# Performance work log

Hardware: AMD Instinct MI355X
Metric: run time of the kernel (lower is better)

## Reference

```python
import jax, jax.numpy as jnp
import numpy as np

USER_NUM = 100000
ITEM_NUM = 50000
EMBED_DIM = 64
N_LAYERS = 2
NNZ_UU, NNZ_UI, NNZ_II = 1600000, 2000000, 800000


def setup_inputs() -> dict:
    key = jax.random.key(0)
    ks = jax.random.split(key, 11)
    return {
        "user_embedding": jax.random.normal(ks[0], (USER_NUM, EMBED_DIM), jnp.float32),
        "item_embedding": jax.random.normal(ks[1], (ITEM_NUM, EMBED_DIM), jnp.float32),
        "uu_val": jax.random.uniform(ks[2], (NNZ_UU,), jnp.float32),
        "ui_val": jax.random.uniform(ks[3], (NNZ_UI,), jnp.float32),
        "ii_val": jax.random.uniform(ks[4], (NNZ_II,), jnp.float32),
        "uu_rows": jax.random.randint(ks[5], (NNZ_UU,), 0, USER_NUM, jnp.int32),
        "uu_cols": jax.random.randint(ks[6], (NNZ_UU,), 0, USER_NUM, jnp.int32),
        "ui_rows": jax.random.randint(ks[7], (NNZ_UI,), 0, USER_NUM, jnp.int32),
        "ui_cols": jax.random.randint(ks[8], (NNZ_UI,), 0, ITEM_NUM, jnp.int32),
        "ii_rows": jax.random.randint(ks[9], (NNZ_II,), 0, ITEM_NUM, jnp.int32),
        "ii_cols": jax.random.randint(ks[10], (NNZ_II,), 0, ITEM_NUM, jnp.int32),
    }


def _spmm(rows, cols, vals, x, n_out):
    # sparse(COO) @ dense: gather source features, scale by edge value, scatter-add to rows
    return jax.ops.segment_sum(vals[:, None] * x[cols], rows, num_segments=n_out)


def reference(user_embedding, item_embedding, uu_val, ui_val, ii_val,
              uu_rows, uu_cols, ui_rows, ui_cols, ii_rows, ii_cols):
    u = user_embedding
    i = item_embedding
    # running sum for mean over (n_layers + 1) layer outputs
    u_sum, i_sum = u, i
    for _ in range(N_LAYERS):
        u_from_i = _spmm(ui_rows, ui_cols, ui_val, i, USER_NUM)        # user_item_graph @ item
        i_from_u = _spmm(ui_cols, ui_rows, ui_val, u, ITEM_NUM)        # user_item_graph.T @ user
        uu = _spmm(uu_rows, uu_cols, uu_val, u, USER_NUM)              # user_graph @ user
        ii = _spmm(ii_rows, ii_cols, ii_val, i, ITEM_NUM)              # item_graph @ item
        u = 0.5 * (uu + u_from_i)   # mean over stacked pair
        i = 0.5 * (ii + i_from_u)
        u_sum = u_sum + u
        i_sum = i_sum + i
    inv = 1.0 / (N_LAYERS + 1)
    return u_sum * inv, i_sum * inv
```

## Files before the change

kernel.cpp:

```cpp
#include <hip/hip_runtime.h>

typedef _Float16 half8_t __attribute__((ext_vector_type(8)));
typedef _Float16 half4_t __attribute__((ext_vector_type(4)));

#define NU 100000
#define NI 50000
#define NR (NU + NI)
#define D 64
#define COARSE 1024
#define RPB 147
#define CAP 8800
#define CHUNK 6144
#define RPT 6
#define RPT2 9
#define NT4 (NR * 16)
#define PKSLACK 448

__global__ void init_kernel(const float4* __restrict__ ue, const float4* __restrict__ ie,
                            half4_t* __restrict__ curh, int* __restrict__ tots) {
    int idx = blockIdx.x * 256 + threadIdx.x;
    if (idx < COARSE) tots[idx] = 0;
    if (idx >= NT4) return;
    float4 v = (idx < NU * 16) ? ue[idx] : ie[idx - NU * 16];
    half4_t h;
    h[0] = (_Float16)v.x; h[1] = (_Float16)v.y; h[2] = (_Float16)v.z; h[3] = (_Float16)v.w;
    curh[idx] = h;
}

__device__ __forceinline__ int place_dest(int p, const int* ui_r, const int* ui_c,
                                          const int* uu_r, const int* ii_r,
                                          int n_ui, int n_uu) {
    if (p < 2 * n_ui) {
        int e = p >> 1;
        return (p & 1) ? NU + ui_c[e] : ui_r[e];
    } else if (p < 2 * n_ui + n_uu) {
        return uu_r[p - 2 * n_ui];
    } else {
        return NU + ii_r[p - 2 * n_ui - n_uu];
    }
}

__global__ void count_kernel(const int* __restrict__ ui_r, const int* __restrict__ ui_c,
                             const int* __restrict__ uu_r, const int* __restrict__ ii_r,
                             int* __restrict__ tots, int n_ui, int n_uu, int nnzt) {
    __shared__ int cnt[COARSE];
    int tid = threadIdx.x;
    cnt[tid] = 0;
    __syncthreads();
    int blk0 = blockIdx.x * CHUNK;
#pragma unroll
    for (int k = 0; k < RPT; k++) {
        int p = blk0 + k * 1024 + tid;
        if (p < nnzt) {
            int dest = place_dest(p, ui_r, ui_c, uu_r, ii_r, n_ui, n_uu);
            atomicAdd(&cnt[dest / RPB], 1);
        }
    }
    __syncthreads();
    if (cnt[tid]) atomicAdd(&tots[tid], cnt[tid]);
}

__global__ void scan1_kernel(const int* __restrict__ tots, int* __restrict__ coarse_base,
                             int* __restrict__ cursor) {
    __shared__ int s[COARSE];
    int tid = threadIdx.x;
    int x = tots[tid];
    s[tid] = x;
    __syncthreads();
    for (int off = 1; off < COARSE; off <<= 1) {
        int t = (tid >= off) ? s[tid - off] : 0;
        __syncthreads();
        s[tid] += t;
        __syncthreads();
    }
    int excl = s[tid] - x;
    coarse_base[tid] = excl;
    cursor[tid] = excl;
    if (tid == COARSE - 1) coarse_base[COARSE] = s[tid];
}

__global__ void place_kernel(const int* __restrict__ ui_r, const int* __restrict__ ui_c,
                             const float* __restrict__ ui_v,
                             const int* __restrict__ uu_r, const int* __restrict__ uu_c,
                             const float* __restrict__ uu_v,
                             const int* __restrict__ ii_r, const int* __restrict__ ii_c,
                             const float* __restrict__ ii_v,
                             int* __restrict__ cursor, uint2* __restrict__ scratch,
                             int n_ui, int n_uu, int nnzt) {
    __shared__ uint2 rec[CHUNK];
    __shared__ int cnt[COARSE];
    __shared__ int lbase[COARSE];
    __shared__ int base_s[COARSE];
    __shared__ int s_ntot;
    int tid = threadIdx.x;
    cnt[tid] = 0;
    __syncthreads();
    int blk0 = blockIdx.x * CHUNK;
    unsigned rk[RPT];
    int sk[RPT];
    unsigned short vk[RPT];
#pragma unroll
    for (int k = 0; k < RPT; k++) {
        int p = blk0 + k * 1024 + tid;
        rk[k] = 0xFFFFFFFFu;
        if (p < nnzt) {
            int dest, src;
            float v;
            if (p < 2 * n_ui) {
                int e = p >> 1;
                int r = ui_r[e], cc = ui_c[e];
                v = ui_v[e];
                if (p & 1) { dest = NU + cc; src = r; }
                else       { dest = r; src = NU + cc; }
            } else if (p < 2 * n_ui + n_uu) {
                int e = p - 2 * n_ui;
                dest = uu_r[e]; src = uu_c[e]; v = uu_v[e];
            } else {
                int e = p - 2 * n_ui - n_uu;
                dest = NU + ii_r[e]; src = NU + ii_c[e]; v = ii_v[e];
            }
            int c = dest / RPB;
            int lr = atomicAdd(&cnt[c], 1);
            int dl = dest - c * RPB;
            rk[k] = ((unsigned)dl << 24) | ((unsigned)c << 14) | (unsigned)lr;
            sk[k] = src;
            _Float16 hv = (_Float16)v;
            __builtin_memcpy(&vk[k], &hv, 2);
        }
    }
    __syncthreads();
    int own = cnt[tid];
    if (own) base_s[tid] = atomicAdd(&cursor[tid], own);
    lbase[tid] = own;
    __syncthreads();
    for (int off = 1; off < COARSE; off <<= 1) {
        int t = (tid >= off) ? lbase[tid - off] : 0;
        __syncthreads();
        lbase[tid] += t;
        __syncthreads();
    }
    int incl = lbase[tid];
    __syncthreads();
    lbase[tid] = incl - own;
    if (tid == COARSE - 1) s_ntot = incl;
    __syncthreads();
#pragma unroll
    for (int k = 0; k < RPT; k++) {
        if (rk[k] == 0xFFFFFFFFu) continue;
        int c  = (rk[k] >> 14) & 0x3FF;
        int lr = rk[k] & 0x3FFF;
        int dl = rk[k] >> 24;
        rec[lbase[c] + lr] = make_uint2(((unsigned)dl << 18) | (unsigned)sk[k],
                                        ((unsigned)c << 16) | (unsigned)vk[k]);
    }
    __syncthreads();
    int ntot = s_ntot;
    for (int i = tid; i < ntot; i += 1024) {
        uint2 r = rec[i];
        int c = r.y >> 16;
        scratch[base_s[c] + (i - lbase[c])] = r;
    }
}

__global__ void csr_kernel(const uint2* __restrict__ scratch, const int* __restrict__ coarse_base,
                           int* __restrict__ ptr, int* __restrict__ pk_src,
                           unsigned short* __restrict__ pk_val) {
    __shared__ int s[1024];
    __shared__ int fine[256];
    __shared__ int fill[256];
    __shared__ int lsrc[CAP];
    __shared__ unsigned short lval[CAP];
    __shared__ int s_pn;
    int c = blockIdx.x, tid = threadIdx.x;
    int rbeg = c * RPB;
    int rcnt = NR - rbeg;
    if (rcnt > RPB) rcnt = RPB;
    if (rcnt < 0) rcnt = 0;
    int base = coarse_base[c], end = coarse_base[c + 1];
    int n = end - base;
    int pkc    = ((base + 3) & ~3) + c * PKSLACK;
    int pknext = ((end  + 3) & ~3) + (c + 1) * PKSLACK;
    bool small = (n <= RPT2 * 1024);
    if (tid < 256) fine[tid] = 0;
    __syncthreads();
    uint2 rc[RPT2];
    if (small) {
#pragma unroll
        for (int k = 0; k < RPT2; k++) {
            int i = k * 1024 + tid;
            if (i < n) {
                rc[k] = scratch[base + i];
                atomicAdd(&fine[rc[k].x >> 18], 1);
            }
        }
    } else {
        for (int i = tid; i < n; i += 1024)
            atomicAdd(&fine[scratch[base + i].x >> 18], 1);
    }
    __syncthreads();
    int own = (tid < 256) ? fine[tid] : 0;
    int own4 = (own + 3) & ~3;
    s[tid] = own4;
    __syncthreads();
    for (int off = 1; off < 256; off <<= 1) {
        int t = (tid >= off) ? s[tid - off] : 0;
        __syncthreads();
        s[tid] += t;
        __syncthreads();
    }
    int excl4 = s[tid] - own4;
    if (tid < rcnt) ptr[rbeg + tid] = pkc + excl4;
    if (tid == 0 && rbeg + rcnt == NR) ptr[NR] = pknext;
    if (tid < 256) fill[tid] = excl4;
    if (tid == 255) s_pn = s[255];
    __syncthreads();
    int pn = s_pn;
    if (small && pn <= CAP) {
        for (int i = tid; i < pn; i += 1024) { lsrc[i] = 0; lval[i] = 0; }
        __syncthreads();
#pragma unroll
        for (int k = 0; k < RPT2; k++) {
            int i = k * 1024 + tid;
            if (i < n) {
                int dl = rc[k].x >> 18;
                int slot = atomicAdd(&fill[dl], 1);
                lsrc[slot] = rc[k].x & 0x3FFFF;
                lval[slot] = (unsigned short)rc[k].y;
            }
        }
        __syncthreads();
        for (int i = tid; i < pn; i += 1024) {
            pk_src[pkc + i] = lsrc[i] << 7;
            pk_val[pkc + i] = lval[i];
        }
        for (int i = pkc + pn + tid; i < pknext; i += 1024) { pk_src[i] = 0; pk_val[i] = 0; }
    } else {
        for (int i = pkc + tid; i < pknext; i += 1024) { pk_src[i] = 0; pk_val[i] = 0; }
        __syncthreads();
        for (int i = tid; i < n; i += 1024) {
            uint2 r2 = scratch[base + i];
            int dl = r2.x >> 18;
            int slot = atomicAdd(&fill[dl], 1);
            pk_src[pkc + slot] = (r2.x & 0x3FFFF) << 7;
            pk_val[pkc + slot] = (unsigned short)r2.y;
        }
    }
}

template<int SV, int SX>
__device__ __forceinline__ void fmamix(float& a, unsigned v, unsigned x) {
    if constexpr (SV == 0 && SX == 0)
        asm("v_fma_mix_f32 %0, %1, %2, %0 op_sel:[0,0,0] op_sel_hi:[1,1,0]"
            : "+v"(a) : "v"(v), "v"(x));
    else if constexpr (SV == 0 && SX == 1)
        asm("v_fma_mix_f32 %0, %1, %2, %0 op_sel:[0,1,0] op_sel_hi:[1,1,0]"
            : "+v"(a) : "v"(v), "v"(x));
    else if constexpr (SV == 1 && SX == 0)
        asm("v_fma_mix_f32 %0, %1, %2, %0 op_sel:[1,0,0] op_sel_hi:[1,1,0]"
            : "+v"(a) : "v"(v), "v"(x));
    else
        asm("v_fma_mix_f32 %0, %1, %2, %0 op_sel:[1,1,0] op_sel_hi:[1,1,0]"
            : "+v"(a) : "v"(v), "v"(x));
}

template<int SV>
__device__ __forceinline__ void edge_fma(float (&acc)[8], unsigned vw, const uint4& x) {
    fmamix<SV, 0>(acc[0], vw, x.x);
    fmamix<SV, 1>(acc[1], vw, x.x);
    fmamix<SV, 0>(acc[2], vw, x.y);
    fmamix<SV, 1>(acc[3], vw, x.y);
    fmamix<SV, 0>(acc[4], vw, x.z);
    fmamix<SV, 1>(acc[5], vw, x.z);
    fmamix<SV, 0>(acc[6], vw, x.w);
    fmamix<SV, 1>(acc[7], vw, x.w);
}

__global__ void spmm_fused(const int* __restrict__ ptr, const int* __restrict__ pk_src,
                           const uint2* __restrict__ pk_val2,
                           const half8_t* __restrict__ src,
                           half8_t* __restrict__ nexth, float4* __restrict__ out,
                           const float4* __restrict__ ue4, const float4* __restrict__ ie4,
                           int layer) {
    int w = (int)((blockIdx.x * blockDim.x + threadIdx.x) >> 6);
    int lane = threadIdx.x & 63;
    if (w >= NR) return;
    int g = lane >> 3;
    int fl = lane & 7;
    int flo = fl << 4;
    const char* sb = (const char*)src;
    const int4* ps = (const int4*)pk_src;

    int b = ptr[w], e = ptr[w + 1];
    int q0 = b >> 2, qe = e >> 2;

    float acc[8];
#pragma unroll
    for (int k = 0; k < 8; k++) acc[k] = 0.f;

    for (int q = q0 + g; q < qe; q += 8) {
        int4 sa = ps[q];
        uint2 va = pk_val2[q];
        uint4 x0 = *(const uint4*)(sb + (sa.x + flo));
        uint4 x1 = *(const uint4*)(sb + (sa.y + flo));
        uint4 x2 = *(const uint4*)(sb + (sa.z + flo));
        uint4 x3 = *(const uint4*)(sb + (sa.w + flo));
        edge_fma<0>(acc, va.x, x0);
        edge_fma<1>(acc, va.x, x1);
        edge_fma<0>(acc, va.y, x2);
        edge_fma<1>(acc, va.y, x3);
    }

#pragma unroll
    for (int k = 0; k < 8; k++) {
        acc[k] += __shfl_xor(acc[k], 8);
        acc[k] += __shfl_xor(acc[k], 16);
        acc[k] += __shfl_xor(acc[k], 32);
    }

    if (lane < 8) {
        float h[8];
#pragma unroll
        for (int k = 0; k < 8; k++) h[k] = 0.5f * acc[k];
        float4* op = out + (size_t)w * 16 + lane * 2;
        if (layer == 0) {
            half8_t hh;
#pragma unroll
            for (int k = 0; k < 8; k++) hh[k] = (_Float16)h[k];
            nexth[w * 8 + lane] = hh;
            op[0] = make_float4(h[0], h[1], h[2], h[3]);
            op[1] = make_float4(h[4], h[5], h[6], h[7]);
        } else {
            const float4* ep = (w < NU) ? (ue4 + (size_t)w * 16 + lane * 2)
                                        : (ie4 + (size_t)(w - NU) * 16 + lane * 2);
            const float inv3 = 1.0f / 3.0f;
            float4 o0 = op[0], o1 = op[1];
            float4 e0 = ep[0], e1 = ep[1];
            o0.x = ((o0.x + e0.x) + h[0]) * inv3;
            o0.y = ((o0.y + e0.y) + h[1]) * inv3;
            o0.z = ((o0.z + e0.z) + h[2]) * inv3;
            o0.w = ((o0.w + e0.w) + h[3]) * inv3;
            o1.x = ((o1.x + e1.x) + h[4]) * inv3;
            o1.y = ((o1.y + e1.y) + h[5]) * inv3;
            o1.z = ((o1.z + e1.z) + h[6]) * inv3;
            o1.w = ((o1.w + e1.w) + h[7]) * inv3;
            op[0] = o0;
            op[1] = o1;
        }
    }
}

extern "C" void kernel_launch(void* const* d_in, const int* in_sizes, int n_in,
                              void* d_out, int out_size, void* d_ws, size_t ws_size,
                              hipStream_t stream) {
    const float* ue      = (const float*)d_in[0];
    const float* ie      = (const float*)d_in[1];
    const float* uu_val  = (const float*)d_in[2];
    const float* ui_val  = (const float*)d_in[3];
    const float* ii_val  = (const float*)d_in[4];
    const int*   uu_rows = (const int*)d_in[5];
    const int*   uu_cols = (const int*)d_in[6];
    const int*   ui_rows = (const int*)d_in[7];
    const int*   ui_cols = (const int*)d_in[8];
    const int*   ii_rows = (const int*)d_in[9];
    const int*   ii_cols = (const int*)d_in[10];

    const int NNZ_UU = in_sizes[2];
    const int NNZ_UI = in_sizes[3];
    const int NNZ_II = in_sizes[4];
    const int NNZT   = 2 * NNZ_UI + NNZ_UU + NNZ_II;
    const int NBLK   = (NNZT + CHUNK - 1) / CHUNK;
    const int PKTOT  = NNZT + PKSLACK * COARSE + 64;

    float* out = (float*)d_out;

    char* wsb = (char*)d_ws;
    half8_t* curh   = (half8_t*)wsb;
    uint2*   scratch = (uint2*)(wsb + (size_t)NR * 128);
    half8_t* nexth  = (half8_t*)scratch;
    int*     pk_src = (int*)(scratch + NNZT);
    unsigned short* pk_val = (unsigned short*)(pk_src + PKTOT);
    int*     ptr    = (int*)(pk_val + PKTOT);
    int*     coarse_base = ptr + (NR + 1);
    int*     tots   = coarse_base + (COARSE + 1);
    int*     cursor = tots + COARSE;

    init_kernel<<<(NT4 + 255) / 256, 256, 0, stream>>>(
        (const float4*)ue, (const float4*)ie, (half4_t*)curh, tots);

    count_kernel<<<NBLK, 1024, 0, stream>>>(
        ui_rows, ui_cols, uu_rows, ii_rows, tots, NNZ_UI, NNZ_UU, NNZT);

    scan1_kernel<<<1, 1024, 0, stream>>>(tots, coarse_base, cursor);

    place_kernel<<<NBLK, 1024, 0, stream>>>(
        ui_rows, ui_cols, ui_val, uu_rows, uu_cols, uu_val,
        ii_rows, ii_cols, ii_val, cursor, scratch, NNZ_UI, NNZ_UU, NNZT);

    csr_kernel<<<COARSE, 1024, 0, stream>>>(scratch, coarse_base, ptr, pk_src, pk_val);

    int blocks = (NR * 64 + 511) / 512;

    spmm_fused<<<blocks, 512, 0, stream>>>(
        ptr, pk_src, (const uint2*)pk_val, curh, nexth, (float4*)out,
        (const float4*)ue, (const float4*)ie, 0);

    spmm_fused<<<blocks, 512, 0, stream>>>(
        ptr, pk_src, (const uint2*)pk_val, nexth, curh, (float4*)out,
        (const float4*)ue, (const float4*)ie, 1);
}
```

Baseline: 471.9 us.

## Replace two-level bucketed CSR build with per-row atomic degree count and scatter

The COO-to-CSR construction drops the coarse-bucket count, scan, local-sort placement and per-bucket CSR kernels. Instead a degree kernel does global atomics per destination row, a single block scans the padded row degrees and zero-fills the padding, and a scatter kernel writes each edge directly to its slot through a per-row atomic cursor. This removes the intermediate scratch pass and two kernels. In exchange it uses many contended global atomics, scatters writes with no locality, and runs the 150k-row scan serially inside one 1024-thread block. Edge order within a row also becomes nondeterministic, which can change floating-point summation order.

New measurement: 1.547 ms. +227.8%, slower.

```diff
diff --git a/kernel.cpp b/kernel.cpp
--- a/kernel.cpp
+++ b/kernel.cpp
@@ -7,19 +7,13 @@
 #define NI 50000
 #define NR (NU + NI)
 #define D 64
-#define COARSE 1024
-#define RPB 147
-#define CAP 8800
-#define CHUNK 6144
-#define RPT 6
-#define RPT2 9
 #define NT4 (NR * 16)
-#define PKSLACK 448
+#define RPS 147
 
 __global__ void init_kernel(const float4* __restrict__ ue, const float4* __restrict__ ie,
-                            half4_t* __restrict__ curh, int* __restrict__ tots) {
+                            half4_t* __restrict__ curh, int* __restrict__ rowdeg) {
     int idx = blockIdx.x * 256 + threadIdx.x;
-    if (idx < COARSE) tots[idx] = 0;
+    if (idx < NR) rowdeg[idx] = 0;
     if (idx >= NT4) return;
     float4 v = (idx < NU * 16) ? ue[idx] : ie[idx - NU * 16];
     half4_t h;
@@ -40,211 +34,78 @@
     }
 }
 
-__global__ void count_kernel(const int* __restrict__ ui_r, const int* __restrict__ ui_c,
-                             const int* __restrict__ uu_r, const int* __restrict__ ii_r,
-                             int* __restrict__ tots, int n_ui, int n_uu, int nnzt) {
-    __shared__ int cnt[COARSE];
+__global__ void degree_kernel(const int* __restrict__ ui_r, const int* __restrict__ ui_c,
+                              const int* __restrict__ uu_r, const int* __restrict__ ii_r,
+                              int* __restrict__ rowdeg, int n_ui, int n_uu, int nnzt) {
+    int p = blockIdx.x * 256 + threadIdx.x;
+    if (p >= nnzt) return;
+    int dest = place_dest(p, ui_r, ui_c, uu_r, ii_r, n_ui, n_uu);
+    atomicAdd(&rowdeg[dest], 1);
+}
+
+__global__ void rowscan_kernel(const int* __restrict__ rowdeg, int* __restrict__ ptr,
+                               int* __restrict__ cursor, int* __restrict__ pk_src,
+                               unsigned short* __restrict__ pk_val) {
+    __shared__ int s[1024];
     int tid = threadIdx.x;
-    cnt[tid] = 0;
+    int r0 = tid * RPS;
+    int r1 = r0 + RPS;
+    if (r1 > NR) r1 = NR;
+    if (r0 > NR) r0 = NR;
+    int sum = 0;
+    for (int r = r0; r < r1; r++) sum += (rowdeg[r] + 3) & ~3;
+    s[tid] = sum;
     __syncthreads();
-    int blk0 = blockIdx.x * CHUNK;
-#pragma unroll
-    for (int k = 0; k < RPT; k++) {
-        int p = blk0 + k * 1024 + tid;
-        if (p < nnzt) {
-            int dest = place_dest(p, ui_r, ui_c, uu_r, ii_r, n_ui, n_uu);
-            atomicAdd(&cnt[dest / RPB], 1);
-        }
-    }
-    __syncthreads();
-    if (cnt[tid]) atomicAdd(&tots[tid], cnt[tid]);
-}
-
-__global__ void scan1_kernel(const int* __restrict__ tots, int* __restrict__ coarse_base,
-                             int* __restrict__ cursor) {
-    __shared__ int s[COARSE];
-    int tid = threadIdx.x;
-    int x = tots[tid];
-    s[tid] = x;
-    __syncthreads();
-    for (int off = 1; off < COARSE; off <<= 1) {
+    for (int off = 1; off < 1024; off <<= 1) {
         int t = (tid >= off) ? s[tid - off] : 0;
         __syncthreads();
         s[tid] += t;
         __syncthreads();
     }
-    int excl = s[tid] - x;
-    coarse_base[tid] = excl;
-    cursor[tid] = excl;
-    if (tid == COARSE - 1) coarse_base[COARSE] = s[tid];
-}
-
-__global__ void place_kernel(const int* __restrict__ ui_r, const int* __restrict__ ui_c,
-                             const float* __restrict__ ui_v,
-                             const int* __restrict__ uu_r, const int* __restrict__ uu_c,
-                             const float* __restrict__ uu_v,
-                             const int* __restrict__ ii_r, const int* __restrict__ ii_c,
-                             const float* __restrict__ ii_v,
-                             int* __restrict__ cursor, uint2* __restrict__ scratch,
-                             int n_ui, int n_uu, int nnzt) {
-    __shared__ uint2 rec[CHUNK];
-    __shared__ int cnt[COARSE];
-    __shared__ int lbase[COARSE];
-    __shared__ int base_s[COARSE];
-    __shared__ int s_ntot;
-    int tid = threadIdx.x;
-    cnt[tid] = 0;
-    __syncthreads();
-    int blk0 = blockIdx.x * CHUNK;
-    unsigned rk[RPT];
-    int sk[RPT];
-    unsigned short vk[RPT];
-#pragma unroll
-    for (int k = 0; k < RPT; k++) {
-        int p = blk0 + k * 1024 + tid;
-        rk[k] = 0xFFFFFFFFu;
-        if (p < nnzt) {
-            int dest, src;
-            float v;
-            if (p < 2 * n_ui) {
-                int e = p >> 1;
-                int r = ui_r[e], cc = ui_c[e];
-                v = ui_v[e];
-                if (p & 1) { dest = NU + cc; src = r; }
-                else       { dest = r; src = NU + cc; }
-            } else if (p < 2 * n_ui + n_uu) {
-                int e = p - 2 * n_ui;
-                dest = uu_r[e]; src = uu_c[e]; v = uu_v[e];
-            } else {
-                int e = p - 2 * n_ui - n_uu;
-                dest = NU + ii_r[e]; src = NU + ii_c[e]; v = ii_v[e];
-            }
-            int c = dest / RPB;
-            int lr = atomicAdd(&cnt[c], 1);
-            int dl = dest - c * RPB;
-            rk[k] = ((unsigned)dl << 24) | ((unsigned)c << 14) | (unsigned)lr;
-            sk[k] = src;
-            _Float16 hv = (_Float16)v;
-            __builtin_memcpy(&vk[k], &hv, 2);
-        }
-    }
-    __syncthreads();
-    int own = cnt[tid];
-    if (own) base_s[tid] = atomicAdd(&cursor[tid], own);
-    lbase[tid] = own;
-    __syncthreads();
-    for (int off = 1; off < COARSE; off <<= 1) {
-        int t = (tid >= off) ? lbase[tid - off] : 0;
-        __syncthreads();
-        lbase[tid] += t;
-        __syncthreads();
-    }
-    int incl = lbase[tid];
-    __syncthreads();
-    lbase[tid] = incl - own;
-    if (tid == COARSE - 1) s_ntot = incl;
-    __syncthreads();
-#pragma unroll
-    for (int k = 0; k < RPT; k++) {
-        if (rk[k] == 0xFFFFFFFFu) continue;
-        int c  = (rk[k] >> 14) & 0x3FF;
-        int lr = rk[k] & 0x3FFF;
-        int dl = rk[k] >> 24;
-        rec[lbase[c] + lr] = make_uint2(((unsigned)dl << 18) | (unsigned)sk[k],
-                                        ((unsigned)c << 16) | (unsigned)vk[k]);
-    }
-    __syncthreads();
-    int ntot = s_ntot;
-    for (int i = tid; i < ntot; i += 1024) {
-        uint2 r = rec[i];
-        int c = r.y >> 16;
-        scratch[base_s[c] + (i - lbase[c])] = r;
-    }
-}
-
-__global__ void csr_kernel(const uint2* __restrict__ scratch, const int* __restrict__ coarse_base,
-                           int* __restrict__ ptr, int* __restrict__ pk_src,
-                           unsigned short* __restrict__ pk_val) {
-    __shared__ int s[1024];
-    __shared__ int fine[256];
-    __shared__ int fill[256];
-    __shared__ int lsrc[CAP];
-    __shared__ unsigned short lval[CAP];
-    __shared__ int s_pn;
-    int c = blockIdx.x, tid = threadIdx.x;
-    int rbeg = c * RPB;
-    int rcnt = NR - rbeg;
-    if (rcnt > RPB) rcnt = RPB;
-    if (rcnt < 0) rcnt = 0;
-    int base = coarse_base[c], end = coarse_base[c + 1];
-    int n = end - base;
-    int pkc    = ((base + 3) & ~3) + c * PKSLACK;
-    int pknext = ((end  + 3) & ~3) + (c + 1) * PKSLACK;
-    bool small = (n <= RPT2 * 1024);
-    if (tid < 256) fine[tid] = 0;
-    __syncthreads();
-    uint2 rc[RPT2];
-    if (small) {
-#pragma unroll
-        for (int k = 0; k < RPT2; k++) {
-            int i = k * 1024 + tid;
-            if (i < n) {
-                rc[k] = scratch[base + i];
-                atomicAdd(&fine[rc[k].x >> 18], 1);
-            }
-        }
+    int run = s[tid] - sum;
+    for (int r = r0; r < r1; r++) {
+        int d = rowdeg[r];
+        int d4 = (d + 3) & ~3;
+        ptr[r] = run;
+        cursor[r] = run;
+        for (int i = run + d; i < run + d4; i++) { pk_src[i] = 0; pk_val[i] = 0; }
+        run += d4;
+    }
+    if (tid == 1023) ptr[NR] = s[1023];
+}
+
+__global__ void scatter_kernel(const int* __restrict__ ui_r, const int* __restrict__ ui_c,
+                               const float* __restrict__ ui_v,
+                               const int* __restrict__ uu_r, const int* __restrict__ uu_c,
+                               const float* __restrict__ uu_v,
+                               const int* __restrict__ ii_r, const int* __restrict__ ii_c,
+                               const float* __restrict__ ii_v,
+                               int* __restrict__ cursor, int* __restrict__ pk_src,
+                               unsigned short* __restrict__ pk_val,
+                               int n_ui, int n_uu, int nnzt) {
+    int p = blockIdx.x * 256 + threadIdx.x;
+    if (p >= nnzt) return;
+    int dest, src;
+    float v;
+    if (p < 2 * n_ui) {
+        int e = p >> 1;
+        int r = ui_r[e], cc = ui_c[e];
+        v = ui_v[e];
+        if (p & 1) { dest = NU + cc; src = r; }
+        else       { dest = r; src = NU + cc; }
+    } else if (p < 2 * n_ui + n_uu) {
+        int e = p - 2 * n_ui;
+        dest = uu_r[e]; src = uu_c[e]; v = uu_v[e];
     } else {
-        for (int i = tid; i < n; i += 1024)
-            atomicAdd(&fine[scratch[base + i].x >> 18], 1);
-    }
-    __syncthreads();
-    int own = (tid < 256) ? fine[tid] : 0;
-    int own4 = (own + 3) & ~3;
-    s[tid] = own4;
-    __syncthreads();
-    for (int off = 1; off < 256; off <<= 1) {
-        int t = (tid >= off) ? s[tid - off] : 0;
-        __syncthreads();
-        s[tid] += t;
-        __syncthreads();
-    }
-    int excl4 = s[tid] - own4;
-    if (tid < rcnt) ptr[rbeg + tid] = pkc + excl4;
-    if (tid == 0 && rbeg + rcnt == NR) ptr[NR] = pknext;
-    if (tid < 256) fill[tid] = excl4;
-    if (tid == 255) s_pn = s[255];
-    __syncthreads();
-    int pn = s_pn;
-    if (small && pn <= CAP) {
-        for (int i = tid; i < pn; i += 1024) { lsrc[i] = 0; lval[i] = 0; }
-        __syncthreads();
-#pragma unroll
-        for (int k = 0; k < RPT2; k++) {
-            int i = k * 1024 + tid;
-            if (i < n) {
-                int dl = rc[k].x >> 18;
-                int slot = atomicAdd(&fill[dl], 1);
-                lsrc[slot] = rc[k].x & 0x3FFFF;
-                lval[slot] = (unsigned short)rc[k].y;
-            }
-        }
-        __syncthreads();
-        for (int i = tid; i < pn; i += 1024) {
-            pk_src[pkc + i] = lsrc[i] << 7;
-            pk_val[pkc + i] = lval[i];
-        }
-        for (int i = pkc + pn + tid; i < pknext; i += 1024) { pk_src[i] = 0; pk_val[i] = 0; }
-    } else {
-        for (int i = pkc + tid; i < pknext; i += 1024) { pk_src[i] = 0; pk_val[i] = 0; }
-        __syncthreads();
-        for (int i = tid; i < n; i += 1024) {
-            uint2 r2 = scratch[base + i];
-            int dl = r2.x >> 18;
-            int slot = atomicAdd(&fill[dl], 1);
-            pk_src[pkc + slot] = (r2.x & 0x3FFFF) << 7;
-            pk_val[pkc + slot] = (unsigned short)r2.y;
-        }
-    }
+        int e = p - 2 * n_ui - n_uu;
+        dest = NU + ii_r[e]; src = NU + ii_c[e]; v = ii_v[e];
+    }
+    int slot = atomicAdd(&cursor[dest], 1);
+    pk_src[slot] = src << 7;
+    _Float16 hv = (_Float16)v;
+    unsigned short us;
+    __builtin_memcpy(&us, &hv, 2);
+    pk_val[slot] = us;
 }
 
 template<int SV, int SX>
@@ -368,35 +229,33 @@
     const int NNZ_UI = in_sizes[3];
     const int NNZ_II = in_sizes[4];
     const int NNZT   = 2 * NNZ_UI + NNZ_UU + NNZ_II;
-    const int NBLK   = (NNZT + CHUNK - 1) / CHUNK;
-    const int PKTOT  = NNZT + PKSLACK * COARSE + 64;
+    int pktot = NNZT + 3 * NR + 16;
+    pktot = (pktot + 3) & ~3;
 
     float* out = (float*)d_out;
 
     char* wsb = (char*)d_ws;
     half8_t* curh   = (half8_t*)wsb;
-    uint2*   scratch = (uint2*)(wsb + (size_t)NR * 128);
-    half8_t* nexth  = (half8_t*)scratch;
-    int*     pk_src = (int*)(scratch + NNZT);
-    unsigned short* pk_val = (unsigned short*)(pk_src + PKTOT);
-    int*     ptr    = (int*)(pk_val + PKTOT);
-    int*     coarse_base = ptr + (NR + 1);
-    int*     tots   = coarse_base + (COARSE + 1);
-    int*     cursor = tots + COARSE;
+    half8_t* nexth  = (half8_t*)(wsb + (size_t)NR * 128);
+    int*     pk_src = (int*)(wsb + (size_t)NR * 256);
+    unsigned short* pk_val = (unsigned short*)(pk_src + pktot);
+    int*     ptr    = (int*)(pk_val + pktot);
+    int*     cursor = ptr + (NR + 1);
+    int*     rowdeg = cursor + NR;
 
     init_kernel<<<(NT4 + 255) / 256, 256, 0, stream>>>(
-        (const float4*)ue, (const float4*)ie, (half4_t*)curh, tots);
-
-    count_kernel<<<NBLK, 1024, 0, stream>>>(
-        ui_rows, ui_cols, uu_rows, ii_rows, tots, NNZ_UI, NNZ_UU, NNZT);
-
-    scan1_kernel<<<1, 1024, 0, stream>>>(tots, coarse_base, cursor);
-
-    place_kernel<<<NBLK, 1024, 0, stream>>>(
+        (const float4*)ue, (const float4*)ie, (half4_t*)curh, rowdeg);
+
+    int pblocks = (NNZT + 255) / 256;
+
+    degree_kernel<<<pblocks, 256, 0, stream>>>(
+        ui_rows, ui_cols, uu_rows, ii_rows, rowdeg, NNZ_UI, NNZ_UU, NNZT);
+
+    rowscan_kernel<<<1, 1024, 0, stream>>>(rowdeg, ptr, cursor, pk_src, pk_val);
+
+    scatter_kernel<<<pblocks, 256, 0, stream>>>(
         ui_rows, ui_cols, ui_val, uu_rows, uu_cols, uu_val,
-        ii_rows, ii_cols, ii_val, cursor, scratch, NNZ_UI, NNZ_UU, NNZT);
-
-    csr_kernel<<<COARSE, 1024, 0, stream>>>(scratch, coarse_base, ptr, pk_src, pk_val);
+        ii_rows, ii_cols, ii_val, cursor, pk_src, pk_val, NNZ_UI, NNZ_UU, NNZT);
 
     int blocks = (NR * 64 + 511) / 512;
 
```
